# Performance work log

Measured on AMD Instinct MI355X. Metric: run time of the kernel, lower is better.

Reference implementation:

```python
import jax, jax.numpy as jnp
import numpy as np

B, L = 32, 200
NUM_C, NUM_D, DIM_V = 256, 32, 128


def setup_inputs() -> dict:
    key = jax.random.key(0)
    ks = jax.random.split(key, 20)
    def n(k, shape, s=0.05):
        return (jax.random.normal(k, shape) * s).astype(jnp.float32)
    return {
        "c_seq": jax.random.randint(ks[0], (B, L), 0, NUM_C),
        "d_seq": jax.random.randint(ks[1], (B, L), 0, NUM_D),
        "r_seq": jax.random.uniform(ks[2], (B, L), dtype=jnp.float32),
        # learned params
        "X": n(ks[3], (NUM_C * NUM_D, DIM_V), 0.1),      # Embedding table
        "v_r": n(ks[4], (DIM_V,), 0.1),
        "v_beta": n(ks[5], (DIM_V,), 0.1),
        # GRU (torch layout: gates [r|z|n] stacked)
        "W_ih": n(ks[6], (3 * DIM_V, 2 * DIM_V)),
        "W_hh": n(ks[7], (3 * DIM_V, DIM_V)),
        "b_ih": n(ks[8], (3 * DIM_V,)),
        "b_hh": n(ks[9], (3 * DIM_V,)),
        # linear_1: dim_v -> dim_v -> num_d (dropout = identity in eval)
        "W1a": n(ks[10], (DIM_V, DIM_V)), "b1a": n(ks[11], (DIM_V,)),
        "W1b": n(ks[12], (NUM_D, DIM_V)), "b1b": n(ks[13], (NUM_D,)),
        # linear_2: 3*dim_v -> dim_v -> num_d
        "W2a": n(ks[14], (DIM_V, 3 * DIM_V)), "b2a": n(ks[15], (DIM_V,)),
        "W2b": n(ks[16], (NUM_D, DIM_V)), "b2b": n(ks[17], (NUM_D,)),
    }


def reference(c_seq, d_seq, r_seq, X, v_r, v_beta, W_ih, W_hh, b_ih, b_hh,
              W1a, b1a, W1b, b1b, W2a, b2a, W2b, b2b):
    # embedding lookup: x = c + num_c * d
    v_x_seq = X[c_seq + NUM_C * d_seq]              # [B,L,V]
    v_r_seq = r_seq[..., None] * v_r                # [B,L,V]
    gru_in = jnp.concatenate([v_x_seq, v_r_seq], -1)  # [B,L,2V]

    # GRU (torch semantics), precompute input projections
    gx = jnp.einsum('blf,gf->blg', gru_in, W_ih) + b_ih  # [B,L,3V]

    def gru_step(h, gx_t):
        gh = h @ W_hh.T + b_hh
        xr, xz, xn = jnp.split(gx_t, 3, axis=-1)
        hr, hz, hn = jnp.split(gh, 3, axis=-1)
        r = jax.nn.sigmoid(xr + hr)
        z = jax.nn.sigmoid(xz + hz)
        n_ = jnp.tanh(xn + r * hn)
        h = (1.0 - z) * n_ + z * h
        return h, h

    h0 = jnp.zeros((B, DIM_V), dtype=gru_in.dtype)
    _, h_seq = jax.lax.scan(gru_step, h0, jnp.swapaxes(gx, 0, 1))
    h_seq = jnp.swapaxes(h_seq, 0, 1)               # [B,L,V]

    # linear_1 (dropout is identity at inference)
    alpha_seq = jax.nn.relu(h_seq @ W1a.T + b1a) @ W1b.T + b1b  # [B,L,num_d]

    # sequential memory update; one-hot gather/scatter expressed as true
    # gather C[b, c_t, d_t] and row scatter C[b, c_t, :] = new_c (same math)
    bidx = jnp.arange(B)

    def mem_step(C, inp):
        c_t, d_t, vx_t, vr_t = inp
        beta = C[bidx, c_t, d_t]                    # [B]
        v_beta_t = beta[:, None] * v_beta           # [B,V]
        zcat = jnp.concatenate([v_beta_t, vx_t, vr_t], -1)  # [B,3V]
        new_c = jax.nn.relu(zcat @ W2a.T + b2a) @ W2b.T + b2b  # [B,num_d]
        C = C.at[bidx, c_t].set(new_c)
        return C, C

    C0 = jnp.zeros((B, NUM_C, NUM_D), jnp.float32)
    _, C_seq = jax.lax.scan(
        mem_step, C0,
        (jnp.swapaxes(c_seq, 0, 1), jnp.swapaxes(d_seq, 0, 1),
         jnp.swapaxes(v_x_seq, 0, 1), jnp.swapaxes(v_r_seq, 0, 1)))
    C_seq = jnp.swapaxes(C_seq, 0, 1)               # [B,L,num_c,num_d]
    return alpha_seq, h_seq, C_seq
```

## Files before the change

kernel.cpp:

```cpp
#include <hip/hip_runtime.h>
#include <hip/hip_bf16.h>

typedef unsigned short u16;
typedef unsigned int u32;
typedef short short8 __attribute__((ext_vector_type(8)));
typedef float f32x4 __attribute__((ext_vector_type(4)));

constexpr int BATCH = 32, L = 200, NUM_C = 256, NUM_D = 32, V = 128;
constexpr int G3 = 384;
constexpr int KQ = 512;
constexpr int ROWS = BATCH * L;
constexpr size_t ALPHA_OFF = 0;
constexpr size_t H_OFF = (size_t)ROWS * NUM_D;
constexpr size_t C_OFF = H_OFF + (size_t)ROWS * V;

__device__ inline u16 f2bf(float f) {
  __hip_bfloat16 h = __float2bfloat16(f);
  return __builtin_bit_cast(u16, h);
}
__device__ inline float bf2f(u16 u) { u32 x = ((u32)u) << 16; return __builtin_bit_cast(float, x); }

__device__ inline void cvt32(const float* __restrict__ src, u16* __restrict__ dst) {
#pragma unroll
  for (int j0 = 0; j0 < 32; j0 += 4) {
    const f32x4 v = *(const f32x4*)(src + j0);
    ushort4 s;
    s.x = f2bf(v[0]); s.y = f2bf(v[1]); s.z = f2bf(v[2]); s.w = f2bf(v[3]);
    *(ushort4*)(dst + j0) = s;
  }
}
__device__ inline short8 ldfrag(const float* __restrict__ p) {
  const f32x4 a = *(const f32x4*)p, b = *(const f32x4*)(p + 4);
  short8 s;
  s[0] = (short)f2bf(a[0]); s[1] = (short)f2bf(a[1]);
  s[2] = (short)f2bf(a[2]); s[3] = (short)f2bf(a[3]);
  s[4] = (short)f2bf(b[0]); s[5] = (short)f2bf(b[1]);
  s[6] = (short)f2bf(b[2]); s[7] = (short)f2bf(b[3]);
  return s;
}

__global__ __launch_bounds__(256) void k1(
    const int* __restrict__ c_seq, const int* __restrict__ d_seq,
    const float* __restrict__ r_seq, const float* __restrict__ X,
    const float* __restrict__ v_r, const float* __restrict__ W_ih,
    const float* __restrict__ W2a, const float* __restrict__ b_ih,
    const float* __restrict__ b2a, float* __restrict__ Qout)
{
  __shared__ __align__(16) u16 Als[64][144];
  __shared__ __align__(16) u16 Bls[64][144];
  const int tid = threadIdx.x;
  const int mt = blockIdx.x, nt = blockIdx.y;
  const int lane = tid & 63, w = tid >> 6;
  const int q = lane >> 4, m = lane & 15;

  f32x4 acc[4];
#pragma unroll
  for (int i = 0; i < 4; ++i) acc[i] = (f32x4)0.0f;

  const int r0 = tid >> 2;
  const int kc = (tid & 3) * 32;
  const int rowg = mt * 64 + r0;
  const int gcolB = nt * 64 + r0;

  for (int s = 0; s < 2; ++s) {
    if (s) __syncthreads();
    if (s == 0) {
      const int idx = c_seq[rowg] + NUM_C * d_seq[rowg];
      cvt32(X + (size_t)idx * V + kc, &Als[r0][kc]);
    } else {
      const float rv = r_seq[rowg];
#pragma unroll
      for (int j0 = 0; j0 < 32; j0 += 4) {
        const f32x4 v = *(const f32x4*)(v_r + kc + j0);
        ushort4 sv;
        sv.x = f2bf(rv * v[0]); sv.y = f2bf(rv * v[1]);
        sv.z = f2bf(rv * v[2]); sv.w = f2bf(rv * v[3]);
        *(ushort4*)&Als[r0][kc + j0] = sv;
      }
    }
    {
      const float* src = (gcolB < G3)
        ? (W_ih + (size_t)gcolB * 256 + s * 128 + kc)
        : (W2a + (size_t)(gcolB - G3) * G3 + V + s * 128 + kc);
      cvt32(src, &Bls[r0][kc]);
    }
    __syncthreads();
#pragma unroll
    for (int c = 0; c < 4; ++c) {
      const short8 af = *(const short8*)&Als[w * 16 + m][32 * c + 8 * q];
#pragma unroll
      for (int i = 0; i < 4; ++i) {
        const short8 bf = *(const short8*)&Bls[i * 16 + m][32 * c + 8 * q];
        acc[i] = __builtin_amdgcn_mfma_f32_16x16x32_bf16(af, bf, acc[i], 0, 0, 0);
      }
    }
  }
#pragma unroll
  for (int i = 0; i < 4; ++i) {
    const int col = nt * 64 + i * 16 + m;
    const float bias = (col < G3) ? b_ih[col] : b2a[col - G3];
#pragma unroll
    for (int r = 0; r < 4; ++r) {
      const int rowo = mt * 64 + w * 16 + q * 4 + r;
      Qout[(size_t)rowo * KQ + col] = acc[i][r] + bias;
    }
  }
}

union ShK2 {
  struct { u16 h_bf[2][V]; } g;
  struct { float C[NUM_C * NUM_D]; int cb[L]; int db[L]; float u[V]; } s;
};

__global__ __launch_bounds__(256) void k2(
    const int* __restrict__ c_seq, const int* __restrict__ d_seq,
    const float* __restrict__ W_hh, const float* __restrict__ b_hh,
    const float* __restrict__ W2a, const float* __restrict__ v_beta,
    const float* __restrict__ W2b, const float* __restrict__ b2b,
    const float* __restrict__ Q, float* __restrict__ out)
{
  __shared__ __align__(16) ShK2 sh;
  const int tid = threadIdx.x;
  const int l = tid & 63, w = tid >> 6, q = l >> 4, m = l & 15;

  if (blockIdx.x < 32) {
    const int b = blockIdx.x;
    if (tid < V) sh.g.h_bf[0][tid] = 0;
    __syncthreads();
    short8 wf[6][4];
    float bhh[6]; int gcol[6];
#pragma unroll
    for (int i = 0; i < 6; ++i) {
      const int g = (w + 4 * i) * 16 + m;
      gcol[i] = g;
      bhh[i] = b_hh[g];
#pragma unroll
      for (int c = 0; c < 4; ++c)
        wf[i][c] = ldfrag(W_hh + (size_t)g * V + 32 * c + 8 * q);
    }
    const float* Qb = Q + (size_t)b * L * KQ;
    float* outh = out + H_OFF + (size_t)b * L * V;
    const int vi0 = 16 * w + m, vi1 = 64 + 16 * w + m;
    float hold[2] = {0.f, 0.f};
    float hst[2] = {0.f, 0.f};
    float gxv[6];
#pragma unroll
    for (int i = 0; i < 6; ++i) gxv[i] = Qb[gcol[i]];
    for (int t = 0; t < L; ++t) {
      const int rs = t & 1, wsl = rs ^ 1;
      float gxn[6];
      const float* Qn = Qb + (size_t)((t + 1 < L) ? t + 1 : t) * KQ;
#pragma unroll
      for (int i = 0; i < 6; ++i) gxn[i] = Qn[gcol[i]];
      if (t > 0 && q == 0) {
        outh[(size_t)(t - 1) * V + vi0] = hst[0];
        outh[(size_t)(t - 1) * V + vi1] = hst[1];
      }
      short8 af[4];
#pragma unroll
      for (int c = 0; c < 4; ++c)
        af[c] = *(const short8*)&sh.g.h_bf[rs][32 * c + 8 * q];
      f32x4 acc[6];
#pragma unroll
      for (int i = 0; i < 6; ++i) acc[i] = (f32x4)0.0f;
#pragma unroll
      for (int c = 0; c < 4; ++c)
#pragma unroll
        for (int i = 0; i < 6; ++i)
          acc[i] = __builtin_amdgcn_mfma_f32_16x16x32_bf16(af[c], wf[i][c], acc[i], 0, 0, 0);
      float hnew[2];
#pragma unroll
      for (int s = 0; s < 2; ++s) {
        const float xr = gxv[0 + s] + acc[0 + s][0] + bhh[0 + s];
        const float xz = gxv[2 + s] + acc[2 + s][0] + bhh[2 + s];
        const float ghn = acc[4 + s][0] + bhh[4 + s];
        const float r = 1.f / (1.f + __expf(-xr));
        const float z = 1.f / (1.f + __expf(-xz));
        const float xn = gxv[4 + s] + r * ghn;
        const float e = __expf(2.f * xn);
        const float n = 1.f - 2.f / (e + 1.f);
        hnew[s] = (1.f - z) * n + z * hold[s];
      }
      if (q == 0) {
        sh.g.h_bf[wsl][vi0] = f2bf(hnew[0]);
        sh.g.h_bf[wsl][vi1] = f2bf(hnew[1]);
      }
      hold[0] = hnew[0]; hold[1] = hnew[1];
      hst[0] = hnew[0]; hst[1] = hnew[1];
      __syncthreads();
#pragma unroll
      for (int i = 0; i < 6; ++i) gxv[i] = gxn[i];
    }
    if (q == 0) {
      outh[(size_t)(L - 1) * V + vi0] = hst[0];
      outh[(size_t)(L - 1) * V + vi1] = hst[1];
    }
  } else {
    const int b = blockIdx.x - 32;
    for (int i = tid; i < NUM_C * NUM_D; i += 256) sh.s.C[i] = 0.f;
    if (tid < L) { sh.s.cb[tid] = c_seq[b * L + tid]; sh.s.db[tid] = d_seq[b * L + tid]; }
    if (tid < V) {
      float a = 0.f;
      const float* wr = W2a + (size_t)tid * G3;
      for (int k = 0; k < V; ++k) a += wr[k] * v_beta[k];
      sh.s.u[tid] = a;
    }
    __syncthreads();
    if (tid >= 64) return;
    float ureg[4][8];
#pragma unroll
    for (int c = 0; c < 4; ++c)
#pragma unroll
      for (int j = 0; j < 8; ++j) ureg[c][j] = sh.s.u[32 * c + 8 * q + j];
    short8 wbf[2][4];
    float bb[2];
#pragma unroll
    for (int tt = 0; tt < 2; ++tt) {
#pragma unroll
      for (int c = 0; c < 4; ++c)
        wbf[tt][c] = ldfrag(W2b + (size_t)(tt * 16 + m) * V + 32 * c + 8 * q);
      bb[tt] = b2b[tt * 16 + m];
    }
    const float* Pb = Q + (size_t)b * L * KQ + G3;
    float* outc = out + C_OFF + (size_t)b * L * (NUM_C * NUM_D);
    f32x4 pcur[4][2];
#pragma unroll
    for (int c = 0; c < 4; ++c) {
      pcur[c][0] = *(const f32x4*)(Pb + 32 * c + 8 * q);
      pcur[c][1] = *(const f32x4*)(Pb + 32 * c + 8 * q + 4);
    }
    float beta = 0.f;
    for (int t = 0; t < L; ++t) {
      const int ct = sh.s.cb[t];
      short8 af[4];
#pragma unroll
      for (int c = 0; c < 4; ++c) {
        short8 a;
#pragma unroll
        for (int j = 0; j < 8; ++j) {
          const float p = (j < 4) ? pcur[c][0][j] : pcur[c][1][j - 4];
          const float hv = fmaxf(beta * ureg[c][j] + p, 0.f);
          a[j] = (short)f2bf(hv);
        }
        af[c] = a;
      }
      const int tn = (t + 1 < L) ? t + 1 : t;
      const float* Pn = Pb + (size_t)tn * KQ;
#pragma unroll
      for (int c = 0; c < 4; ++c) {
        pcur[c][0] = *(const f32x4*)(Pn + 32 * c + 8 * q);
        pcur[c][1] = *(const f32x4*)(Pn + 32 * c + 8 * q + 4);
      }
      f32x4 a0 = (f32x4)0.0f, a1 = (f32x4)0.0f;
#pragma unroll
      for (int c = 0; c < 4; ++c) {
        a0 = __builtin_amdgcn_mfma_f32_16x16x32_bf16(af[c], wbf[0][c], a0, 0, 0, 0);
        a1 = __builtin_amdgcn_mfma_f32_16x16x32_bf16(af[c], wbf[1][c], a1, 0, 0, 0);
      }
      const float n0 = a0[0] + bb[0], n1 = a1[0] + bb[1];
      if (q == 0) {
        sh.s.C[ct * NUM_D + m] = n0;
        sh.s.C[ct * NUM_D + 16 + m] = n1;
        float* oc = outc + (size_t)t * (NUM_C * NUM_D) + ct * NUM_D;
        oc[m] = n0;
        oc[16 + m] = n1;
      }
      __builtin_amdgcn_s_waitcnt(0xc07f);
      if (t + 1 < L)
        beta = sh.s.C[sh.s.cb[t + 1] * NUM_D + sh.s.db[t + 1]];
    }
  }
}

union ShK3 {
  struct { int cb[L]; float stage[L][NUM_D]; } f;
  struct { u16 hls[64][144]; u16 hid[64][144]; } a;
};

__global__ __launch_bounds__(256) void k3(
    const int* __restrict__ c_seq, const float* __restrict__ W1a,
    const float* __restrict__ b1a, const float* __restrict__ W1b,
    const float* __restrict__ b1b, float* __restrict__ out)
{
  __shared__ __align__(16) ShK3 sh;
  const int tid = threadIdx.x;
  if (blockIdx.x < 256) {
    const int blk = blockIdx.x;
    const int b = blk >> 3, cbase = (blk & 7) * 32;
    if (tid < L) sh.f.cb[tid] = c_seq[b * L + tid];
    __syncthreads();
    if (tid < L) {
      const int c = sh.f.cb[tid];
      if (c >= cbase && c < cbase + 32) {
        const float* src = out + C_OFF + ((size_t)b * L + tid) * (NUM_C * NUM_D) + (size_t)c * NUM_D;
#pragma unroll
        for (int j = 0; j < 8; ++j)
          *(f32x4*)&sh.f.stage[tid][j * 4] = *(const f32x4*)(src + j * 4);
      }
    }
    __syncthreads();
    const int cl = tid >> 3, dq = (tid & 7) * 4;
    const int myc = cbase + cl;
    float* base = out + C_OFF + (size_t)b * L * (NUM_C * NUM_D) + (size_t)myc * NUM_D + dq;
    f32x4 cur = (f32x4)0.0f;
    for (int t = 0; t < L; ++t) {
      if (sh.f.cb[t] == myc) cur = *(const f32x4*)&sh.f.stage[t][dq];
      *(f32x4*)base = cur;
      base += NUM_C * NUM_D;
    }
  } else {
    const int ab = blockIdx.x - 256;
    const int l = tid & 63, w = tid >> 6, q = l >> 4, m = l & 15;
    {
      const int r0 = tid >> 2, kc = (tid & 3) * 32;
      cvt32(out + H_OFF + (size_t)(ab * 64 + r0) * V + kc, &sh.a.hls[r0][kc]);
    }
    __syncthreads();
    f32x4 acc1[8];
#pragma unroll
    for (int i = 0; i < 8; ++i) acc1[i] = (f32x4)0.0f;
#pragma unroll
    for (int c = 0; c < 4; ++c) {
      const short8 af = *(const short8*)&sh.a.hls[w * 16 + m][32 * c + 8 * q];
#pragma unroll
      for (int i = 0; i < 8; ++i) {
        const short8 bf = ldfrag(W1a + (size_t)(i * 16 + m) * V + 32 * c + 8 * q);
        acc1[i] = __builtin_amdgcn_mfma_f32_16x16x32_bf16(af, bf, acc1[i], 0, 0, 0);
      }
    }
#pragma unroll
    for (int i = 0; i < 8; ++i) {
      const int col = i * 16 + m;
      const float bias = b1a[col];
#pragma unroll
      for (int r = 0; r < 4; ++r)
        sh.a.hid[w * 16 + q * 4 + r][col] = f2bf(fmaxf(acc1[i][r] + bias, 0.f));
    }
    __syncthreads();
    f32x4 acc2[2];
    acc2[0] = (f32x4)0.0f; acc2[1] = (f32x4)0.0f;
#pragma unroll
    for (int c = 0; c < 4; ++c) {
      const short8 af = *(const short8*)&sh.a.hid[w * 16 + m][32 * c + 8 * q];
#pragma unroll
      for (int tt = 0; tt < 2; ++tt) {
        const short8 bf = ldfrag(W1b + (size_t)(tt * 16 + m) * V + 32 * c + 8 * q);
        acc2[tt] = __builtin_amdgcn_mfma_f32_16x16x32_bf16(af, bf, acc2[tt], 0, 0, 0);
      }
    }
#pragma unroll
    for (int tt = 0; tt < 2; ++tt) {
      const int col = tt * 16 + m;
      const float bias = b1b[col];
#pragma unroll
      for (int r = 0; r < 4; ++r) {
        const int row = ab * 64 + w * 16 + q * 4 + r;
        out[ALPHA_OFF + (size_t)row * NUM_D + col] = acc2[tt][r] + bias;
      }
    }
  }
}

extern "C" void kernel_launch(void* const* d_in, const int* in_sizes, int n_in,
                              void* d_out, int out_size, void* d_ws, size_t ws_size,
                              hipStream_t stream) {
  const int*   c_seq  = (const int*)d_in[0];
  const int*   d_seq  = (const int*)d_in[1];
  const float* r_seq  = (const float*)d_in[2];
  const float* X      = (const float*)d_in[3];
  const float* v_r    = (const float*)d_in[4];
  const float* v_beta = (const float*)d_in[5];
  const float* W_ih   = (const float*)d_in[6];
  const float* W_hh   = (const float*)d_in[7];
  const float* b_ih   = (const float*)d_in[8];
  const float* b_hh   = (const float*)d_in[9];
  const float* W1a    = (const float*)d_in[10];
  const float* b1a    = (const float*)d_in[11];
  const float* W1b    = (const float*)d_in[12];
  const float* b1b    = (const float*)d_in[13];
  const float* W2a    = (const float*)d_in[14];
  const float* b2a    = (const float*)d_in[15];
  const float* W2b    = (const float*)d_in[16];
  const float* b2b    = (const float*)d_in[17];
  float* out = (float*)d_out;
  float* Q = (float*)d_ws;

  k1<<<dim3(100, 8), 256, 0, stream>>>(c_seq, d_seq, r_seq, X, v_r, W_ih, W2a, b_ih, b2a, Q);
  k2<<<64, 256, 0, stream>>>(c_seq, d_seq, W_hh, b_hh, W2a, v_beta, W2b, b2b, Q, out);
  k3<<<356, 256, 0, stream>>>(c_seq, W1a, b1a, W1b, b1b, out);
}
```

Measured before the change: 399.3 us.

## Deepen GRU gx prefetch, forward beta via bpermute, truncate bf16 packing

In the GRU recurrence, gate inputs are now prefetched two steps ahead, and the full __syncthreads is replaced by an LDS-only waitcnt plus a raw barrier, so global loads can stay in flight across steps. In the memory-update scan, the next beta is read from shared memory early. When the next concept equals the current one, beta is instead forwarded from the freshly computed outputs with ds_bpermute, which removes the store-then-reload dependency through LDS. The bf16 conversion switches from round-to-nearest to truncating bit packing, which slightly changes numerics.

```diff
diff --git a/kernel.cpp b/kernel.cpp
--- a/kernel.cpp
+++ b/kernel.cpp
@@ -143,15 +143,18 @@
     const int vi0 = 16 * w + m, vi1 = 64 + 16 * w + m;
     float hold[2] = {0.f, 0.f};
     float hst[2] = {0.f, 0.f};
-    float gxv[6];
+    float gxv[6], gxn[6];
 #pragma unroll
     for (int i = 0; i < 6; ++i) gxv[i] = Qb[gcol[i]];
+#pragma unroll
+    for (int i = 0; i < 6; ++i) gxn[i] = Qb[KQ + gcol[i]];
     for (int t = 0; t < L; ++t) {
       const int rs = t & 1, wsl = rs ^ 1;
-      float gxn[6];
-      const float* Qn = Qb + (size_t)((t + 1 < L) ? t + 1 : t) * KQ;
-#pragma unroll
-      for (int i = 0; i < 6; ++i) gxn[i] = Qn[gcol[i]];
+      float gx2[6];
+      const int t2 = (t + 2 < L) ? t + 2 : L - 1;
+      const float* Q2 = Qb + (size_t)t2 * KQ;
+#pragma unroll
+      for (int i = 0; i < 6; ++i) gx2[i] = Q2[gcol[i]];
       if (t > 0 && q == 0) {
         outh[(size_t)(t - 1) * V + vi0] = hst[0];
         outh[(size_t)(t - 1) * V + vi1] = hst[1];
@@ -187,9 +190,10 @@
       }
       hold[0] = hnew[0]; hold[1] = hnew[1];
       hst[0] = hnew[0]; hst[1] = hnew[1];
-      __syncthreads();
-#pragma unroll
-      for (int i = 0; i < 6; ++i) gxv[i] = gxn[i];
+      __builtin_amdgcn_s_waitcnt(0xc07f);
+      __builtin_amdgcn_s_barrier();
+#pragma unroll
+      for (int i = 0; i < 6; ++i) { gxv[i] = gxn[i]; gxn[i] = gx2[i]; }
     }
     if (q == 0) {
       outh[(size_t)(L - 1) * V + vi0] = hst[0];
@@ -230,21 +234,27 @@
       pcur[c][1] = *(const f32x4*)(Pb + 32 * c + 8 * q + 4);
     }
     float beta = 0.f;
+    int ct = sh.s.cb[0];
     for (int t = 0; t < L; ++t) {
-      const int ct = sh.s.cb[t];
+      const int tn = (t + 1 < L) ? t + 1 : t;
+      const int ct1 = sh.s.cb[tn], d1 = sh.s.db[tn];
+      const float beta_old = sh.s.C[ct1 * NUM_D + d1];
       short8 af[4];
 #pragma unroll
       for (int c = 0; c < 4; ++c) {
-        short8 a;
-#pragma unroll
-        for (int j = 0; j < 8; ++j) {
-          const float p = (j < 4) ? pcur[c][0][j] : pcur[c][1][j - 4];
-          const float hv = fmaxf(beta * ureg[c][j] + p, 0.f);
-          a[j] = (short)f2bf(hv);
+        u32 wv[4];
+#pragma unroll
+        for (int jp = 0; jp < 4; ++jp) {
+          const float p0 = (jp < 2) ? pcur[c][0][2 * jp] : pcur[c][1][2 * jp - 4];
+          const float p1 = (jp < 2) ? pcur[c][0][2 * jp + 1] : pcur[c][1][2 * jp - 3];
+          const float h0 = fmaxf(fmaf(beta, ureg[c][2 * jp], p0), 0.f);
+          const float h1 = fmaxf(fmaf(beta, ureg[c][2 * jp + 1], p1), 0.f);
+          wv[jp] = (__builtin_bit_cast(u32, h1) & 0xffff0000u) |
+                   (__builtin_bit_cast(u32, h0) >> 16);
         }
-        af[c] = a;
-      }
-      const int tn = (t + 1 < L) ? t + 1 : t;
+        const uint4 u4 = {wv[0], wv[1], wv[2], wv[3]};
+        af[c] = __builtin_bit_cast(short8, u4);
+      }
       const float* Pn = Pb + (size_t)tn * KQ;
 #pragma unroll
       for (int c = 0; c < 4; ++c) {
@@ -265,9 +275,12 @@
         oc[m] = n0;
         oc[16 + m] = n1;
       }
-      __builtin_amdgcn_s_waitcnt(0xc07f);
-      if (t + 1 < L)
-        beta = sh.s.C[sh.s.cb[t + 1] * NUM_D + sh.s.db[t + 1]];
+      const float nsel = (d1 < 16) ? n0 : n1;
+      const int bp = __builtin_amdgcn_ds_bpermute(
+          (d1 & 15) * 4, __builtin_bit_cast(int, nsel));
+      const float beta_fwd = __builtin_bit_cast(float, bp);
+      beta = (ct1 == ct) ? beta_fwd : beta_old;
+      ct = ct1;
     }
   }
 }
```

After: 415.1 us. 4.0% more time.
